# Performance work log

Hardware: AMD Instinct MI355X
Metric: run time of the kernel (lower is better)

The kernel has to match this reference:

```python
import jax, jax.numpy as jnp
import numpy as np

EMBED_DIM = 256
EPS = 1e-5  # torch F.instance_norm default eps


def setup_inputs() -> dict:
    key = jax.random.key(0)
    ks = jax.random.split(key, 11)
    B, Nq, Nm, C = 4, 4096, 4096, EMBED_DIM
    s = 1.0 / np.sqrt(C)
    return {
        "query": jax.random.normal(ks[0], (B, Nq, C), jnp.float32),
        "key": jax.random.normal(ks[1], (B, Nm, C), jnp.float32),
        "value": jax.random.normal(ks[2], (B, Nm, C), jnp.float32),
        "Wq": jax.random.normal(ks[3], (C, C), jnp.float32) * s,
        "bq": jnp.zeros((C,), jnp.float32),
        "Wk": jax.random.normal(ks[4], (C, C), jnp.float32) * s,
        "bk": jnp.zeros((C,), jnp.float32),
        "Wv": jax.random.normal(ks[5], (C, C), jnp.float32) * s,
        "bv": jnp.zeros((C,), jnp.float32),
        "Wm": jax.random.normal(ks[6], (C, C), jnp.float32) * s,
        "bm": jnp.zeros((C,), jnp.float32),
    }


def reference(query, key, value, Wq, bq, Wk, bk, Wv, bv, Wm, bm):
    # Linear projections (torch nn.Linear: x @ W.T + b)
    q = query @ Wq.T + bq   # [B, Nq, C]
    k = key @ Wk.T + bk     # [B, Nm, C]
    v = value @ Wv.T + bv   # [B, Nm, C]

    attn = jnp.einsum('bnc,bmc->bnm', q, k)  # [B, Nq, Nm]

    # F.instance_norm on [B, Nq, Nm]: N=B, C=Nq, spatial=Nm -> normalize each
    # row over the last dim with biased variance, eps=1e-5, no affine.
    mu = jnp.mean(attn, axis=-1, keepdims=True)
    var = jnp.mean(jnp.square(attn - mu), axis=-1, keepdims=True)
    attn = (attn - mu) * jax.lax.rsqrt(var + EPS)

    # use_softmax=True branch
    attn = attn * (EMBED_DIM ** -0.5)
    attn = jax.nn.softmax(attn, axis=-1)

    out = jnp.einsum('bnm,bmc->bnc', attn, v)  # [B, Nq, C]

    # add_residual=True branch
    return (query + out) @ Wm.T + bm
```

## Files before the change

kernel.cpp:

```cpp
#include <hip/hip_runtime.h>
#include <hip/hip_bf16.h>
#include <cmath>

#define CD 256
#define NQ 4096
#define NM 4096
#define NB 4
#define NTOT (NB*NQ)

typedef __bf16 bf16;
typedef __attribute__((ext_vector_type(8))) __bf16 bf16x8;
typedef __attribute__((ext_vector_type(4))) __bf16 bf16x4;
typedef __attribute__((ext_vector_type(4))) float f32x4;

#define MFMA(a,b,c) __builtin_amdgcn_mfma_f32_16x16x32_bf16(a,b,c,0,0,0)

__global__ __launch_bounds__(256) void cvt_w_kernel(
    const float* __restrict__ wq, const float* __restrict__ wk,
    const float* __restrict__ wv, const float* __restrict__ wm,
    bf16* __restrict__ out)
{
    int i = (blockIdx.x*256 + threadIdx.x)*4;
    const float* srcs[4] = {wq, wk, wv, wm};
    #pragma unroll
    for (int m=0;m<4;++m){
        f32x4 v = *(const f32x4*)(srcs[m]+i);
        bf16x4 o;
        #pragma unroll
        for (int e=0;e<4;++e) o[e] = (bf16)v[e];
        *(bf16x4*)(out + m*65536 + i) = o;
    }
}

template<int MODE>
__global__ __launch_bounds__(256) void proj_kernel(
    const float* __restrict__ X, const bf16* __restrict__ W,
    const float* __restrict__ bias, bf16* __restrict__ out)
{
    const int wave = threadIdx.x>>6, lane = threadIdx.x&63;
    const int lr = lane&15, lg = lane>>4;
    const int n0 = (blockIdx.x>>2)*64 + wave*16;
    const int co0 = (blockIdx.x&3)*64;

    bf16x8 xf[8];
    {
        const float* xr = X + (size_t)(n0+lr)*CD + lg*8;
        #pragma unroll
        for (int ch=0; ch<8; ++ch){
            f32x4 a = *(const f32x4*)(xr + ch*32);
            f32x4 b = *(const f32x4*)(xr + ch*32 + 4);
            bf16x8 t;
            #pragma unroll
            for (int e=0;e<4;++e){ t[e]=(bf16)a[e]; t[4+e]=(bf16)b[e]; }
            xf[ch]=t;
        }
    }
    f32x4 acc[4];
    #pragma unroll
    for (int t=0;t<4;++t) acc[t]=(f32x4){0,0,0,0};

    #pragma unroll
    for (int t=0;t<4;++t){
        const bf16* wr = W + (size_t)(co0+t*16+lr)*CD + lg*8;
        #pragma unroll
        for (int ch=0; ch<8; ++ch){
            bf16x8 wf = *(const bf16x8*)(wr + ch*32);
            if (MODE==0) acc[t] = MFMA(wf, xf[ch], acc[t]);
            else         acc[t] = MFMA(xf[ch], wf, acc[t]);
        }
    }

    if (MODE==0){
        const int n = n0 + lr;
        #pragma unroll
        for (int t=0;t<4;++t){
            int co = co0 + t*16 + 4*lg;
            bf16x4 o;
            #pragma unroll
            for (int r=0;r<4;++r) o[r] = (bf16)(acc[t][r] + bias[co+r]);
            *(bf16x4*)(out + (size_t)n*CD + co) = o;
        }
    } else {
        const int b = n0 / NM;
        const int m0 = (n0 % NM) + 4*lg;
        #pragma unroll
        for (int t=0;t<4;++t){
            int co = co0 + t*16 + lr;
            float bb = bias[co];
            bf16x4 o;
            #pragma unroll
            for (int r=0;r<4;++r) o[r] = (bf16)(acc[t][r] + bb);
            *(bf16x4*)(out + (size_t)b*CD*NM + (size_t)co*NM + m0) = o;
        }
    }
}

__global__ __launch_bounds__(256) void ksum_kernel(
    const bf16* __restrict__ kt, float* __restrict__ ksum)
{
    const int wave = threadIdx.x>>6, lane = threadIdx.x&63;
    const int b = blockIdx.x>>6, c = (blockIdx.x&63)*4 + wave;
    const bf16* row = kt + (size_t)b*CD*NM + (size_t)c*NM;
    float s = 0.0f;
    #pragma unroll
    for (int i=0;i<8;++i){
        bf16x8 v = *(const bf16x8*)(row + (i*64+lane)*8);
        #pragma unroll
        for (int e=0;e<8;++e) s += (float)v[e];
    }
    #pragma unroll
    for (int off=1; off<64; off<<=1) s += __shfl_xor(s, off);
    if (lane==0) ksum[b*256 + c] = s;
}

__global__ __launch_bounds__(256) void gram_kernel(
    const bf16* __restrict__ kt, float* __restrict__ gpart)
{
    const int wave = threadIdx.x>>6, lane = threadIdx.x&63;
    const int lr = lane&15, lg = lane>>4;
    const int b = blockIdx.x>>5, ct = (blockIdx.x>>3)&3, jc = blockIdx.x&7;
    const bf16* ktb = kt + (size_t)b*CD*NM;
    const int c0 = ct*64 + wave*16;

    f32x4 acc[16];
    #pragma unroll
    for (int t=0;t<16;++t) acc[t]=(f32x4){0,0,0,0};

    for (int it=0; it<16; ++it){
        const int j0 = jc*512 + it*32;
        bf16x8 af = *(const bf16x8*)(ktb + (size_t)(c0+lr)*NM + j0 + lg*8);
        #pragma unroll
        for (int t=0;t<16;++t){
            bf16x8 bfr = *(const bf16x8*)(ktb + (size_t)(t*16+lr)*NM + j0 + lg*8);
            acc[t] = MFMA(af, bfr, acc[t]);
        }
    }
    #pragma unroll
    for (int t=0;t<16;++t){
        #pragma unroll
        for (int r=0;r<4;++r){
            int c  = c0 + 4*lg + r;
            int cp = t*16 + lr;
            gpart[(((size_t)jc*4 + b)*256 + c)*256 + cp] = acc[t][r];
        }
    }
}

__global__ __launch_bounds__(256) void gfin_kernel(
    const float* __restrict__ gpart, bf16* __restrict__ gbf)
{
    int gid = blockIdx.x*256 + threadIdx.x;
    int b = gid>>16, idx = gid&65535;
    float s = 0.0f;
    #pragma unroll
    for (int jc=0;jc<8;++jc) s += gpart[((size_t)jc*4 + b)*65536 + idx];
    gbf[(size_t)b*65536 + idx] = (bf16)s;
}

__global__ __launch_bounds__(256) void rowstats_kernel(
    const bf16* __restrict__ q, const bf16* __restrict__ gbf,
    const float* __restrict__ ksumg, float* __restrict__ stats)
{
    __shared__ float ksum[256];
    const int wave = threadIdx.x>>6, lane = threadIdx.x&63;
    const int lr = lane&15, lg = lane>>4;
    const int n0 = blockIdx.x*64;
    const int b = n0 / NQ;
    const int row16 = n0 + wave*16;
    ksum[threadIdx.x] = ksumg[b*256 + threadIdx.x];
    __syncthreads();

    bf16x8 qf[8];
    const bf16* qr = q + (size_t)(row16+lr)*CD + lg*8;
    #pragma unroll
    for (int ch=0; ch<8; ++ch) qf[ch] = *(const bf16x8*)(qr + ch*32);

    const bf16* gb = gbf + (size_t)b*65536;
    f32x4 acc[16];
    #pragma unroll
    for (int t=0;t<16;++t) acc[t]=(f32x4){0,0,0,0};
    #pragma unroll
    for (int t=0;t<16;++t){
        #pragma unroll
        for (int ch=0; ch<8; ++ch){
            bf16x8 bf = *(const bf16x8*)&gb[(size_t)(t*16+lr)*256 + ch*32 + lg*8];
            acc[t] = MFMA(qf[ch], bf, acc[t]);
        }
    }
    float msq[4]={0,0,0,0}, mean[4]={0,0,0,0};
    #pragma unroll
    for (int t=0;t<16;++t){
        float ks = ksum[t*16+lr];
        #pragma unroll
        for (int r=0;r<4;++r){
            float qv = (float)q[(size_t)(row16+4*lg+r)*CD + t*16+lr];
            msq[r]  = fmaf(acc[t][r], qv, msq[r]);
            mean[r] = fmaf(qv, ks, mean[r]);
        }
    }
    #pragma unroll
    for (int off=1; off<16; off<<=1){
        #pragma unroll
        for (int r=0;r<4;++r){
            msq[r]  += __shfl_xor(msq[r], off);
            mean[r] += __shfl_xor(mean[r], off);
        }
    }
    if (lr==0){
        #pragma unroll
        for (int r=0;r<4;++r){
            int row = row16 + 4*lg + r;
            float mu = mean[r]*(1.0f/NM);
            float ms = msq[r]*(1.0f/NM);
            float var = ms - mu*mu;
            float rstd = rsqrtf(fmaxf(var,0.0f) + 1e-5f);
            float a2 = rstd * (1.0f/16.0f) * 1.4426950408889634f;
            stats[row*2+0] = mu*a2;
            stats[row*2+1] = a2;
        }
    }
}

__global__ __launch_bounds__(512) void flash_kernel(
    const bf16* __restrict__ q, const bf16* __restrict__ k,
    const bf16* __restrict__ vt, const float* __restrict__ stats,
    bf16* __restrict__ opart, float* __restrict__ dpart)
{
    __shared__ __align__(16) bf16 K_lds[32][264];
    __shared__ __align__(16) bf16 P_lds[128][40];
    const int wave = threadIdx.x>>6, lane = threadIdx.x&63;
    const int lr = lane&15, lg = lane>>4;
    const int qt = blockIdx.x>>2, slice = blockIdx.x&3;
    const int n0 = qt*128;
    const int b = n0 / NQ;
    const bf16* kb = k  + (size_t)b*NM*CD;
    const bf16* vb = vt + (size_t)b*CD*NM + (size_t)(wave*32)*NM;
    const int row16 = n0 + wave*16;

    bf16x8 qf[8];
    const bf16* qr = q + (size_t)(row16+lr)*CD + lg*8;
    #pragma unroll
    for (int ch=0; ch<8; ++ch) qf[ch] = *(const bf16x8*)(qr + ch*32);

    float c2r[4], a2r[4];
    #pragma unroll
    for (int r=0;r<4;++r){
        int row = row16 + 4*lg + r;
        c2r[r] = stats[row*2+0];
        a2r[r] = stats[row*2+1];
    }

    f32x4 oacc[8][2];
    #pragma unroll
    for (int rt=0;rt<8;++rt){ oacc[rt][0]=(f32x4){0,0,0,0}; oacc[rt][1]=(f32x4){0,0,0,0}; }
    float denom[4]={0,0,0,0};

    const int jbeg = slice*(NM/4);
    bf16x8 kreg0, kreg1;
    {
        int f0 = threadIdx.x, f1 = threadIdx.x + 512;
        kreg0 = *(const bf16x8*)(kb + (size_t)(jbeg + (f0>>5))*CD + (f0&31)*8);
        kreg1 = *(const bf16x8*)(kb + (size_t)(jbeg + (f1>>5))*CD + (f1&31)*8);
    }
    for (int it=0; it<32; ++it){
        const int j0 = jbeg + it*32;
        {
            int f0 = threadIdx.x, f1 = threadIdx.x + 512;
            *(bf16x8*)&K_lds[f0>>5][(f0&31)*8] = kreg0;
            *(bf16x8*)&K_lds[f1>>5][(f1&31)*8] = kreg1;
        }
        __syncthreads();
        if (it < 31){
            int f0 = threadIdx.x, f1 = threadIdx.x + 512;
            kreg0 = *(const bf16x8*)(kb + (size_t)(j0+32 + (f0>>5))*CD + (f0&31)*8);
            kreg1 = *(const bf16x8*)(kb + (size_t)(j0+32 + (f1>>5))*CD + (f1&31)*8);
        }
        f32x4 s0=(f32x4){0,0,0,0}, s1=(f32x4){0,0,0,0};
        #pragma unroll
        for (int ch=0; ch<8; ++ch){
            s0 = MFMA(qf[ch], *(const bf16x8*)&K_lds[lr][lg*8+ch*32], s0);
            s1 = MFMA(qf[ch], *(const bf16x8*)&K_lds[16+lr][lg*8+ch*32], s1);
        }
        #pragma unroll
        for (int r=0;r<4;++r){
            float p0 = exp2f(s0[r]*a2r[r] - c2r[r]);
            float p1 = exp2f(s1[r]*a2r[r] - c2r[r]);
            denom[r] += p0 + p1;
            P_lds[wave*16+4*lg+r][lr]    = (bf16)p0;
            P_lds[wave*16+4*lg+r][16+lr] = (bf16)p1;
        }
        __syncthreads();
        bf16x8 vf0 = *(const bf16x8*)(vb + (size_t)lr*NM      + j0 + lg*8);
        bf16x8 vf1 = *(const bf16x8*)(vb + (size_t)(16+lr)*NM + j0 + lg*8);
        #pragma unroll
        for (int rt=0;rt<8;++rt){
            bf16x8 pf = *(const bf16x8*)&P_lds[rt*16+lr][lg*8];
            oacc[rt][0] = MFMA(pf, vf0, oacc[rt][0]);
            oacc[rt][1] = MFMA(pf, vf1, oacc[rt][1]);
        }
    }

    #pragma unroll
    for (int off=1; off<16; off<<=1){
        #pragma unroll
        for (int r=0;r<4;++r) denom[r] += __shfl_xor(denom[r], off);
    }
    if (lr==0){
        #pragma unroll
        for (int r=0;r<4;++r)
            dpart[(size_t)slice*NTOT + row16 + 4*lg + r] = denom[r];
    }
    #pragma unroll
    for (int rt=0;rt<8;++rt){
        #pragma unroll
        for (int ct=0;ct<2;++ct){
            #pragma unroll
            for (int r=0;r<4;++r){
                int row = n0 + rt*16 + 4*lg + r;
                int co  = wave*32 + ct*16 + lr;
                opart[((size_t)slice*NTOT + row)*CD + co] = (bf16)oacc[rt][ct][r];
            }
        }
    }
}

__global__ __launch_bounds__(256) void combine_kernel(
    const bf16* __restrict__ opart, const float* __restrict__ dpart,
    const float* __restrict__ query, bf16* __restrict__ u)
{
    int gid = blockIdx.x*256 + threadIdx.x;
    int row = gid>>5, c0 = (gid&31)*8;
    float dsum = dpart[row] + dpart[NTOT+row] + dpart[2*NTOT+row] + dpart[3*(size_t)NTOT+row];
    float inv = 1.0f/dsum;
    float acc[8]={0,0,0,0,0,0,0,0};
    #pragma unroll
    for (int s=0;s<4;++s){
        bf16x8 o = *(const bf16x8*)&opart[((size_t)s*NTOT+row)*CD + c0];
        #pragma unroll
        for (int e=0;e<8;++e) acc[e] += (float)o[e];
    }
    f32x4 qa = *(const f32x4*)(query + (size_t)row*CD + c0);
    f32x4 qb = *(const f32x4*)(query + (size_t)row*CD + c0 + 4);
    bf16x8 out;
    #pragma unroll
    for (int e=0;e<4;++e){
        out[e]   = (bf16)(qa[e] + acc[e]*inv);
        out[4+e] = (bf16)(qb[e] + acc[4+e]*inv);
    }
    *(bf16x8*)&u[(size_t)row*CD + c0] = out;
}

__global__ __launch_bounds__(256) void final_kernel(
    const bf16* __restrict__ U, const bf16* __restrict__ W,
    const float* __restrict__ bias, float* __restrict__ out)
{
    const int wave = threadIdx.x>>6, lane = threadIdx.x&63;
    const int lr = lane&15, lg = lane>>4;
    const int n0 = (blockIdx.x>>2)*64 + wave*16;
    const int co0 = (blockIdx.x&3)*64;

    bf16x8 uf[8];
    const bf16* ur = U + (size_t)(n0+lr)*CD + lg*8;
    #pragma unroll
    for (int ch=0; ch<8; ++ch) uf[ch] = *(const bf16x8*)(ur + ch*32);

    f32x4 acc[4];
    #pragma unroll
    for (int t=0;t<4;++t) acc[t]=(f32x4){0,0,0,0};

    #pragma unroll
    for (int t=0;t<4;++t){
        const bf16* wr = W + (size_t)(co0+t*16+lr)*CD + lg*8;
        #pragma unroll
        for (int ch=0; ch<8; ++ch)
            acc[t] = MFMA(*(const bf16x8*)(wr+ch*32), uf[ch], acc[t]);
    }
    const int n = n0 + lr;
    #pragma unroll
    for (int t=0;t<4;++t){
        int co = co0 + t*16 + 4*lg;
        f32x4 o;
        #pragma unroll
        for (int r=0;r<4;++r) o[r] = acc[t][r] + bias[co+r];
        *(f32x4*)(out + (size_t)n*CD + co) = o;
    }
}

extern "C" void kernel_launch(void* const* d_in, const int* in_sizes, int n_in,
                              void* d_out, int out_size, void* d_ws, size_t ws_size,
                              hipStream_t stream)
{
    const float* query = (const float*)d_in[0];
    const float* key_  = (const float*)d_in[1];
    const float* value = (const float*)d_in[2];
    const float* Wq = (const float*)d_in[3];
    const float* bq = (const float*)d_in[4];
    const float* Wk = (const float*)d_in[5];
    const float* bk = (const float*)d_in[6];
    const float* Wv = (const float*)d_in[7];
    const float* bv = (const float*)d_in[8];
    const float* Wm = (const float*)d_in[9];
    const float* bm = (const float*)d_in[10];
    float* out = (float*)d_out;

    bf16* wsb = (bf16*)d_ws;
    bf16* wqb = wsb;
    bf16* wkb = wqb + 65536;
    bf16* wvb = wkb + 65536;
    bf16* wmb = wvb + 65536;
    bf16* qbuf  = wsb + 4*65536;
    bf16* kbuf  = qbuf  + (size_t)NTOT*CD;
    bf16* vtbuf = kbuf  + (size_t)NTOT*CD;
    float* statsbuf = (float*)(vtbuf + (size_t)NTOT*CD);
    float* ksumbuf  = statsbuf + (size_t)NTOT*2;
    bf16*  gbf      = (bf16*)(ksumbuf + 1024);
    float* dpart    = (float*)(gbf + (size_t)4*65536);
    bf16*  opart    = (bf16*)(dpart + (size_t)NTOT*4);
    bf16*  ktbuf    = opart;
    float* gpart    = (float*)(opart + (size_t)4*NTOT*CD);
    bf16*  ubuf     = (bf16*)gpart;

    cvt_w_kernel<<<64,256,0,stream>>>(Wq, Wk, Wv, Wm, wsb);
    proj_kernel<0><<<1024,256,0,stream>>>(query, wqb, bq, qbuf);
    proj_kernel<0><<<1024,256,0,stream>>>(key_,  wkb, bk, kbuf);
    proj_kernel<1><<<1024,256,0,stream>>>(key_,  wkb, bk, ktbuf);
    proj_kernel<1><<<1024,256,0,stream>>>(value, wvb, bv, vtbuf);
    ksum_kernel<<<256,256,0,stream>>>(ktbuf, ksumbuf);
    gram_kernel<<<128,256,0,stream>>>(ktbuf, gpart);
    gfin_kernel<<<1024,256,0,stream>>>(gpart, gbf);
    rowstats_kernel<<<256,256,0,stream>>>(qbuf, gbf, ksumbuf, statsbuf);
    flash_kernel<<<512,512,0,stream>>>(qbuf, kbuf, vtbuf, statsbuf, opart, dpart);
    combine_kernel<<<2048,256,0,stream>>>(opart, dpart, query, ubuf);
    final_kernel<<<1024,256,0,stream>>>(ubuf, wmb, bm, out);
}
```

Measured before the change: 415.6 us.

## Fuse K projections, widen flash key tile to 64, fold combine into final GEMM

The two key projections (row-major and transposed) are merged into one kernel, so the key input is read and converted once. The flash kernel now processes 64 keys per iteration instead of 32, which halves the barrier and loop count per block but uses more LDS and registers. The combine kernel is replaced by a tiny per-row reciprocal kernel. The partial-output reduction and residual add now happen inside the final projection GEMM, which removes the intermediate u buffer round trip. In exchange, the final kernel reads the four opart slices for every column tile.

```diff
diff --git a/kernel.cpp b/kernel.cpp
--- a/kernel.cpp
+++ b/kernel.cpp
@@ -35,7 +35,7 @@
 template<int MODE>
 __global__ __launch_bounds__(256) void proj_kernel(
     const float* __restrict__ X, const bf16* __restrict__ W,
-    const float* __restrict__ bias, bf16* __restrict__ out)
+    const float* __restrict__ bias, bf16* __restrict__ out, bf16* __restrict__ out2)
 {
     const int wave = threadIdx.x>>6, lane = threadIdx.x&63;
     const int lr = lane&15, lg = lane>>4;
@@ -55,9 +55,9 @@
             xf[ch]=t;
         }
     }
-    f32x4 acc[4];
-    #pragma unroll
-    for (int t=0;t<4;++t) acc[t]=(f32x4){0,0,0,0};
+    f32x4 acc[4], acc2[4];
+    #pragma unroll
+    for (int t=0;t<4;++t){ acc[t]=(f32x4){0,0,0,0}; acc2[t]=(f32x4){0,0,0,0}; }
 
     #pragma unroll
     for (int t=0;t<4;++t){
@@ -65,12 +65,14 @@
         #pragma unroll
         for (int ch=0; ch<8; ++ch){
             bf16x8 wf = *(const bf16x8*)(wr + ch*32);
-            if (MODE==0) acc[t] = MFMA(wf, xf[ch], acc[t]);
-            else         acc[t] = MFMA(xf[ch], wf, acc[t]);
-        }
-    }
-
-    if (MODE==0){
+            if (MODE==0)      acc[t]  = MFMA(wf, xf[ch], acc[t]);
+            else if (MODE==1) acc2[t] = MFMA(xf[ch], wf, acc2[t]);
+            else {            acc[t]  = MFMA(wf, xf[ch], acc[t]);
+                              acc2[t] = MFMA(xf[ch], wf, acc2[t]); }
+        }
+    }
+
+    if (MODE==0 || MODE==2){
         const int n = n0 + lr;
         #pragma unroll
         for (int t=0;t<4;++t){
@@ -80,7 +82,8 @@
             for (int r=0;r<4;++r) o[r] = (bf16)(acc[t][r] + bias[co+r]);
             *(bf16x4*)(out + (size_t)n*CD + co) = o;
         }
-    } else {
+    }
+    if (MODE==1 || MODE==2){
         const int b = n0 / NM;
         const int m0 = (n0 % NM) + 4*lg;
         #pragma unroll
@@ -89,8 +92,8 @@
             float bb = bias[co];
             bf16x4 o;
             #pragma unroll
-            for (int r=0;r<4;++r) o[r] = (bf16)(acc[t][r] + bb);
-            *(bf16x4*)(out + (size_t)b*CD*NM + (size_t)co*NM + m0) = o;
+            for (int r=0;r<4;++r) o[r] = (bf16)(acc2[t][r] + bb);
+            *(bf16x4*)(out2 + (size_t)b*CD*NM + (size_t)co*NM + m0) = o;
         }
     }
 }
@@ -226,8 +229,8 @@
     const bf16* __restrict__ vt, const float* __restrict__ stats,
     bf16* __restrict__ opart, float* __restrict__ dpart)
 {
-    __shared__ __align__(16) bf16 K_lds[32][264];
-    __shared__ __align__(16) bf16 P_lds[128][40];
+    __shared__ __align__(16) bf16 K_lds[64][264];
+    __shared__ __align__(16) bf16 P_lds[128][72];
     const int wave = threadIdx.x>>6, lane = threadIdx.x&63;
     const int lr = lane&15, lg = lane>>4;
     const int qt = blockIdx.x>>2, slice = blockIdx.x&3;
@@ -256,47 +259,60 @@
     float denom[4]={0,0,0,0};
 
     const int jbeg = slice*(NM/4);
-    bf16x8 kreg0, kreg1;
-    {
-        int f0 = threadIdx.x, f1 = threadIdx.x + 512;
-        kreg0 = *(const bf16x8*)(kb + (size_t)(jbeg + (f0>>5))*CD + (f0&31)*8);
-        kreg1 = *(const bf16x8*)(kb + (size_t)(jbeg + (f1>>5))*CD + (f1&31)*8);
-    }
-    for (int it=0; it<32; ++it){
-        const int j0 = jbeg + it*32;
-        {
-            int f0 = threadIdx.x, f1 = threadIdx.x + 512;
-            *(bf16x8*)&K_lds[f0>>5][(f0&31)*8] = kreg0;
-            *(bf16x8*)&K_lds[f1>>5][(f1&31)*8] = kreg1;
+    bf16x8 kreg[4];
+    #pragma unroll
+    for (int p=0;p<4;++p){
+        int f = threadIdx.x + p*512;
+        kreg[p] = *(const bf16x8*)(kb + (size_t)(jbeg + (f>>5))*CD + (f&31)*8);
+    }
+    for (int it=0; it<16; ++it){
+        const int j0 = jbeg + it*64;
+        #pragma unroll
+        for (int p=0;p<4;++p){
+            int f = threadIdx.x + p*512;
+            *(bf16x8*)&K_lds[f>>5][(f&31)*8] = kreg[p];
         }
         __syncthreads();
-        if (it < 31){
-            int f0 = threadIdx.x, f1 = threadIdx.x + 512;
-            kreg0 = *(const bf16x8*)(kb + (size_t)(j0+32 + (f0>>5))*CD + (f0&31)*8);
-            kreg1 = *(const bf16x8*)(kb + (size_t)(j0+32 + (f1>>5))*CD + (f1&31)*8);
+        if (it < 15){
+            #pragma unroll
+            for (int p=0;p<4;++p){
+                int f = threadIdx.x + p*512;
+                kreg[p] = *(const bf16x8*)(kb + (size_t)(j0+64 + (f>>5))*CD + (f&31)*8);
+            }
         }
         f32x4 s0=(f32x4){0,0,0,0}, s1=(f32x4){0,0,0,0};
+        f32x4 s2=(f32x4){0,0,0,0}, s3=(f32x4){0,0,0,0};
         #pragma unroll
         for (int ch=0; ch<8; ++ch){
-            s0 = MFMA(qf[ch], *(const bf16x8*)&K_lds[lr][lg*8+ch*32], s0);
+            s0 = MFMA(qf[ch], *(const bf16x8*)&K_lds[     lr][lg*8+ch*32], s0);
             s1 = MFMA(qf[ch], *(const bf16x8*)&K_lds[16+lr][lg*8+ch*32], s1);
+            s2 = MFMA(qf[ch], *(const bf16x8*)&K_lds[32+lr][lg*8+ch*32], s2);
+            s3 = MFMA(qf[ch], *(const bf16x8*)&K_lds[48+lr][lg*8+ch*32], s3);
         }
         #pragma unroll
         for (int r=0;r<4;++r){
             float p0 = exp2f(s0[r]*a2r[r] - c2r[r]);
             float p1 = exp2f(s1[r]*a2r[r] - c2r[r]);
-            denom[r] += p0 + p1;
-            P_lds[wave*16+4*lg+r][lr]    = (bf16)p0;
-            P_lds[wave*16+4*lg+r][16+lr] = (bf16)p1;
+            float p2 = exp2f(s2[r]*a2r[r] - c2r[r]);
+            float p3 = exp2f(s3[r]*a2r[r] - c2r[r]);
+            denom[r] += (p0 + p1) + (p2 + p3);
+            int prow = wave*16 + 4*lg + r;
+            P_lds[prow][lr]    = (bf16)p0;
+            P_lds[prow][16+lr] = (bf16)p1;
+            P_lds[prow][32+lr] = (bf16)p2;
+            P_lds[prow][48+lr] = (bf16)p3;
         }
         __syncthreads();
-        bf16x8 vf0 = *(const bf16x8*)(vb + (size_t)lr*NM      + j0 + lg*8);
-        bf16x8 vf1 = *(const bf16x8*)(vb + (size_t)(16+lr)*NM + j0 + lg*8);
-        #pragma unroll
-        for (int rt=0;rt<8;++rt){
-            bf16x8 pf = *(const bf16x8*)&P_lds[rt*16+lr][lg*8];
-            oacc[rt][0] = MFMA(pf, vf0, oacc[rt][0]);
-            oacc[rt][1] = MFMA(pf, vf1, oacc[rt][1]);
+        #pragma unroll
+        for (int w=0; w<2; ++w){
+            bf16x8 vf0 = *(const bf16x8*)(vb + (size_t)lr*NM      + j0 + w*32 + lg*8);
+            bf16x8 vf1 = *(const bf16x8*)(vb + (size_t)(16+lr)*NM + j0 + w*32 + lg*8);
+            #pragma unroll
+            for (int rt=0;rt<8;++rt){
+                bf16x8 pf = *(const bf16x8*)&P_lds[rt*16+lr][w*32+lg*8];
+                oacc[rt][0] = MFMA(pf, vf0, oacc[rt][0]);
+                oacc[rt][1] = MFMA(pf, vf1, oacc[rt][1]);
+            }
         }
     }
 
@@ -324,50 +340,50 @@
     }
 }
 
-__global__ __launch_bounds__(256) void combine_kernel(
-    const bf16* __restrict__ opart, const float* __restrict__ dpart,
-    const float* __restrict__ query, bf16* __restrict__ u)
-{
-    int gid = blockIdx.x*256 + threadIdx.x;
-    int row = gid>>5, c0 = (gid&31)*8;
-    float dsum = dpart[row] + dpart[NTOT+row] + dpart[2*NTOT+row] + dpart[3*(size_t)NTOT+row];
-    float inv = 1.0f/dsum;
-    float acc[8]={0,0,0,0,0,0,0,0};
-    #pragma unroll
-    for (int s=0;s<4;++s){
-        bf16x8 o = *(const bf16x8*)&opart[((size_t)s*NTOT+row)*CD + c0];
-        #pragma unroll
-        for (int e=0;e<8;++e) acc[e] += (float)o[e];
-    }
-    f32x4 qa = *(const f32x4*)(query + (size_t)row*CD + c0);
-    f32x4 qb = *(const f32x4*)(query + (size_t)row*CD + c0 + 4);
-    bf16x8 out;
-    #pragma unroll
-    for (int e=0;e<4;++e){
-        out[e]   = (bf16)(qa[e] + acc[e]*inv);
-        out[4+e] = (bf16)(qb[e] + acc[4+e]*inv);
-    }
-    *(bf16x8*)&u[(size_t)row*CD + c0] = out;
+__global__ __launch_bounds__(256) void dinv_kernel(
+    const float* __restrict__ dpart, float* __restrict__ dinv)
+{
+    int row = blockIdx.x*256 + threadIdx.x;
+    dinv[row] = 1.0f / (dpart[row] + dpart[NTOT+row]
+                      + dpart[2*(size_t)NTOT+row] + dpart[3*(size_t)NTOT+row]);
 }
 
 __global__ __launch_bounds__(256) void final_kernel(
-    const bf16* __restrict__ U, const bf16* __restrict__ W,
+    const bf16* __restrict__ opart, const float* __restrict__ dinv,
+    const float* __restrict__ query, const bf16* __restrict__ W,
     const float* __restrict__ bias, float* __restrict__ out)
 {
     const int wave = threadIdx.x>>6, lane = threadIdx.x&63;
     const int lr = lane&15, lg = lane>>4;
     const int n0 = (blockIdx.x>>2)*64 + wave*16;
     const int co0 = (blockIdx.x&3)*64;
+    const int n = n0 + lr;
+    const float di = dinv[n];
 
     bf16x8 uf[8];
-    const bf16* ur = U + (size_t)(n0+lr)*CD + lg*8;
-    #pragma unroll
-    for (int ch=0; ch<8; ++ch) uf[ch] = *(const bf16x8*)(ur + ch*32);
+    #pragma unroll
+    for (int ch=0; ch<8; ++ch){
+        const int c = lg*8 + ch*32;
+        float a[8];
+        f32x4 qa = *(const f32x4*)(query + (size_t)n*CD + c);
+        f32x4 qb = *(const f32x4*)(query + (size_t)n*CD + c + 4);
+        #pragma unroll
+        for (int e=0;e<4;++e){ a[e]=qa[e]; a[4+e]=qb[e]; }
+        #pragma unroll
+        for (int s=0;s<4;++s){
+            bf16x8 o = *(const bf16x8*)&opart[((size_t)s*NTOT + n)*CD + c];
+            #pragma unroll
+            for (int e=0;e<8;++e) a[e] = fmaf((float)o[e], di, a[e]);
+        }
+        bf16x8 t;
+        #pragma unroll
+        for (int e=0;e<8;++e) t[e] = (bf16)a[e];
+        uf[ch] = t;
+    }
 
     f32x4 acc[4];
     #pragma unroll
     for (int t=0;t<4;++t) acc[t]=(f32x4){0,0,0,0};
-
     #pragma unroll
     for (int t=0;t<4;++t){
         const bf16* wr = W + (size_t)(co0+t*16+lr)*CD + lg*8;
@@ -375,7 +391,6 @@
         for (int ch=0; ch<8; ++ch)
             acc[t] = MFMA(*(const bf16x8*)(wr+ch*32), uf[ch], acc[t]);
     }
-    const int n = n0 + lr;
     #pragma unroll
     for (int t=0;t<4;++t){
         int co = co0 + t*16 + 4*lg;
@@ -413,23 +428,22 @@
     bf16* vtbuf = kbuf  + (size_t)NTOT*CD;
     float* statsbuf = (float*)(vtbuf + (size_t)NTOT*CD);
     float* ksumbuf  = statsbuf + (size_t)NTOT*2;
-    bf16*  gbf      = (bf16*)(ksumbuf + 1024);
+    float* dinvbuf  = ksumbuf + 1024;
+    bf16*  gbf      = (bf16*)(dinvbuf + NTOT);
     float* dpart    = (float*)(gbf + (size_t)4*65536);
     bf16*  opart    = (bf16*)(dpart + (size_t)NTOT*4);
     bf16*  ktbuf    = opart;
     float* gpart    = (float*)(opart + (size_t)4*NTOT*CD);
-    bf16*  ubuf     = (bf16*)gpart;
 
     cvt_w_kernel<<<64,256,0,stream>>>(Wq, Wk, Wv, Wm, wsb);
-    proj_kernel<0><<<1024,256,0,stream>>>(query, wqb, bq, qbuf);
-    proj_kernel<0><<<1024,256,0,stream>>>(key_,  wkb, bk, kbuf);
-    proj_kernel<1><<<1024,256,0,stream>>>(key_,  wkb, bk, ktbuf);
-    proj_kernel<1><<<1024,256,0,stream>>>(value, wvb, bv, vtbuf);
+    proj_kernel<0><<<1024,256,0,stream>>>(query, wqb, bq, qbuf,  nullptr);
+    proj_kernel<2><<<1024,256,0,stream>>>(key_,  wkb, bk, kbuf,  ktbuf);
+    proj_kernel<1><<<1024,256,0,stream>>>(value, wvb, bv, nullptr, vtbuf);
     ksum_kernel<<<256,256,0,stream>>>(ktbuf, ksumbuf);
     gram_kernel<<<128,256,0,stream>>>(ktbuf, gpart);
     gfin_kernel<<<1024,256,0,stream>>>(gpart, gbf);
     rowstats_kernel<<<256,256,0,stream>>>(qbuf, gbf, ksumbuf, statsbuf);
     flash_kernel<<<512,512,0,stream>>>(qbuf, kbuf, vtbuf, statsbuf, opart, dpart);
-    combine_kernel<<<2048,256,0,stream>>>(opart, dpart, query, ubuf);
-    final_kernel<<<1024,256,0,stream>>>(ubuf, wmb, bm, out);
-}
+    dinv_kernel<<<64,256,0,stream>>>(dpart, dinvbuf);
+    final_kernel<<<1024,256,0,stream>>>(opart, dinvbuf, query, wmb, bm, out);
+}
```

New measurement: 407.1 us. -2.0%, faster.
